# Optimization experiments

Hardware: AMD Instinct MI355X
Metric: run time of the kernel (lower is better)

Reference implementation:

```python
import jax, jax.numpy as jnp
import numpy as np

B, S, H = 2, 2048, 2048
N_HEADS = 16
HEAD_DIM = H // N_HEADS


def setup_inputs() -> dict:
    key = jax.random.key(0)
    ks = jax.random.split(key, 9)
    s = 1.0 / np.sqrt(H)
    inp = {
        "x": jax.random.normal(ks[0], (B, S, H), dtype=jnp.float32),
        "wq": jax.random.uniform(ks[1], (H, H), jnp.float32, -s, s),
        "bq": jnp.zeros((H,), jnp.float32),
        "wk": jax.random.uniform(ks[2], (H, H), jnp.float32, -s, s),
        "bk": jnp.zeros((H,), jnp.float32),
        "wv": jax.random.uniform(ks[3], (H, H), jnp.float32, -s, s),
        "bv": jnp.zeros((H,), jnp.float32),
        "wo": jax.random.uniform(ks[4], (H, H), jnp.float32, -s, s),
        "bo": jnp.zeros((H,), jnp.float32),
    }
    return inp


def reference(x, wq, bq, wk, bk, wv, bv, wo, bo):
    bsz, seq_len, hidden = x.shape
    scale = HEAD_DIM ** -0.5
    # projections -> [b, h, s, d]
    def proj(w, b):
        y = jnp.einsum("bsh,oh->bso", x, w) + b
        return y.reshape(bsz, seq_len, N_HEADS, HEAD_DIM).transpose(0, 2, 1, 3)
    q = proj(wq, bq)
    k = proj(wk, bk)
    v = proj(wv, bv)
    scores = jnp.einsum("bhqd,bhkd->bhqk", q, k) * scale
    causal = jnp.tril(jnp.ones((seq_len, seq_len), dtype=bool))
    scores = jnp.where(causal, scores, -jnp.inf)
    attn = jax.nn.softmax(scores, axis=-1)
    out = jnp.einsum("bhqk,bhkd->bhqd", attn, v)
    out = out.transpose(0, 2, 1, 3).reshape(bsz, seq_len, hidden)
    return jnp.einsum("bsh,oh->bso", out, wo) + bo
```

## Files before the change

kernel.cpp:

```cpp
#include <hip/hip_runtime.h>
#include <hip/hip_bf16.h>
#include <cstdint>
#include <cstddef>

#define BATCH 2
#define S_LEN 2048
#define HID   2048
#define NH    16
#define HD    128
#define GK    2048
#define NT    (GK / 64)
#define NIT   (NT / 2)
#define ATT_TILES (32 * NH * BATCH)

typedef short bf16x8 __attribute__((ext_vector_type(8)));
typedef float f32x4  __attribute__((ext_vector_type(4)));

__device__ inline unsigned short f2bf(float f) {
    unsigned int u = __float_as_uint(f);
    unsigned int r = (u + 0x7fffu + ((u >> 16) & 1u)) >> 16;
    return (unsigned short)r;
}

__global__ __launch_bounds__(256) void conv_f32_bf16(const float* __restrict__ src,
                                                     unsigned short* __restrict__ dst,
                                                     long n) {
    long i = ((long)blockIdx.x * 256 + threadIdx.x) * 8;
    if (i >= n) return;
    const float4 a = *(const float4*)(src + i);
    const float4 b = *(const float4*)(src + i + 4);
    union { unsigned short u[8]; bf16x8 v; } o;
    o.u[0] = f2bf(a.x); o.u[1] = f2bf(a.y); o.u[2] = f2bf(a.z); o.u[3] = f2bf(a.w);
    o.u[4] = f2bf(b.x); o.u[5] = f2bf(b.y); o.u[6] = f2bf(b.z); o.u[7] = f2bf(b.w);
    *(bf16x8*)(dst + i) = o.v;
}

__global__ __launch_bounds__(256) void conv4_f32_bf16(const float* __restrict__ s0,
                                                      const float* __restrict__ s1,
                                                      const float* __restrict__ s2,
                                                      const float* __restrict__ s3,
                                                      unsigned short* __restrict__ d0,
                                                      unsigned short* __restrict__ d1,
                                                      unsigned short* __restrict__ d2,
                                                      unsigned short* __restrict__ d3,
                                                      long n) {
    const int z = blockIdx.y;
    const float* src = (z == 0) ? s0 : (z == 1) ? s1 : (z == 2) ? s2 : s3;
    unsigned short* dst = (z == 0) ? d0 : (z == 1) ? d1 : (z == 2) ? d2 : d3;
    long i = ((long)blockIdx.x * 256 + threadIdx.x) * 8;
    if (i >= n) return;
    const float4 a = *(const float4*)(src + i);
    const float4 b = *(const float4*)(src + i + 4);
    union { unsigned short u[8]; bf16x8 v; } o;
    o.u[0] = f2bf(a.x); o.u[1] = f2bf(a.y); o.u[2] = f2bf(a.z); o.u[3] = f2bf(a.w);
    o.u[4] = f2bf(b.x); o.u[5] = f2bf(b.y); o.u[6] = f2bf(b.z); o.u[7] = f2bf(b.w);
    *(bf16x8*)(dst + i) = o.v;
}

__global__ void zero_int(int* p) { *p = 0; }


#define STAGE(DU, SRC, KT, H) do {                                            \
    const unsigned short* _s0 = (SRC) + (size_t)((H) * 128) * GK + (KT) * 64; \
    __builtin_amdgcn_global_load_lds(                                         \
        (const __attribute__((address_space(1))) void*)_s0,                   \
        (__attribute__((address_space(3))) void*)(Sm + (DU) + (H) * 8192 + sdst), \
        16, 0, 0);                                                            \
    __builtin_amdgcn_global_load_lds(                                         \
        (const __attribute__((address_space(1))) void*)(_s0 + (size_t)64 * GK), \
        (__attribute__((address_space(3))) void*)(Sm + (DU) + (H) * 8192 + 4096 + sdst), \
        16, 0, 0);                                                            \
} while (0)

#define READ_AF(D, AB) do { _Pragma("unroll")                                 \
    for (int mi = 0; mi < 4; ++mi) {                                          \
        const int r_ = wm * 64 + mi * 16 + ln;                                \
        AB[mi][0] = *(const bf16x8*)&Sm[(D) * 24576 + r_ * 64 + sw0];         \
        AB[mi][1] = *(const bf16x8*)&Sm[(D) * 24576 + r_ * 64 + sw1];         \
    } } while (0)

#define READ_BH(D, BB, HH) do { _Pragma("unroll")                             \
    for (int ni = 0; ni < 2; ++ni) {                                          \
        const int r_ = wn * 64 + ((HH) * 2 + ni) * 16 + ln;                   \
        BB[ni][0] = *(const bf16x8*)&Sm[(D) * 24576 + 16384 + r_ * 64 + sw0]; \
        BB[ni][1] = *(const bf16x8*)&Sm[(D) * 24576 + 16384 + r_ * 64 + sw1]; \
    } } while (0)

#define MFMA_H(AB, BB, HH) do { _Pragma("unroll")                             \
    for (int mi = 0; mi < 4; ++mi) _Pragma("unroll")                          \
    for (int ni = 0; ni < 2; ++ni) _Pragma("unroll")                          \
    for (int ks = 0; ks < 2; ++ks)                                            \
        acc[mi][(HH)*2+ni] = __builtin_amdgcn_mfma_f32_16x16x32_bf16(         \
            AB[mi][ks], BB[ni][ks], acc[mi][(HH)*2+ni], 0, 0, 0);             \
} while (0)

#define PRIO1 __builtin_amdgcn_s_setprio(1)
#define PRIO0 __builtin_amdgcn_s_setprio(0)
#define BAR   __builtin_amdgcn_s_barrier()
#define VM0   asm volatile("s_waitcnt vmcnt(0)" ::: "memory")

__device__ __forceinline__ void gemm256_core(const unsigned short* __restrict__ A,
                                             const unsigned short* __restrict__ Bw,
                                             const float* __restrict__ bias,
                                             void* __restrict__ Cout,
                                             int mode, int M0, int N0,
                                             unsigned short* Sm) {
    const int tid  = threadIdx.x;
    const int lane = tid & 63;
    const int wave = tid >> 6;
    const int ln = lane & 15, g = lane >> 4;
    const int wm = wave & 3, wn = wave >> 2;

    const int strow = tid >> 3;
    const int stcol = (((tid & 7) ^ ((tid >> 3) & 7)) << 3);
    const unsigned short* gA = A  + (size_t)(M0 + strow) * GK + stcol;
    const unsigned short* gB = Bw + (size_t)(N0 + strow) * GK + stcol;
    const int sdst = wave * 512;

    const int sw0 = ((g    ) ^ (ln & 7)) << 3;
    const int sw1 = ((g + 4) ^ (ln & 7)) << 3;

    f32x4 acc[4][4];
#pragma unroll
    for (int i = 0; i < 4; ++i)
#pragma unroll
        for (int j = 0; j < 4; ++j) acc[i][j] = (f32x4){0.f, 0.f, 0.f, 0.f};
    bf16x8 aE[4][2], aO[4][2], bA[2][2], bB[2][2];

    STAGE(0,     gA, 0, 0); STAGE(0,     gA, 0, 1);
    STAGE(16384, gB, 0, 0);
    STAGE(24576, gA, 1, 0); STAGE(24576, gA, 1, 1);
    asm volatile("s_waitcnt vmcnt(4)" ::: "memory");
    BAR;
    READ_AF(0, aE); READ_BH(0, bA, 0);

    for (int it = 0; it < NIT; ++it) {
        const int kt1 = 2 * it + 1;
        const int kt2 = (2 * it + 2 < NT) ? 2 * it + 2 : NT - 1;
        const int kt3 = (2 * it + 3 < NT) ? 2 * it + 3 : NT - 1;
        BAR;
        STAGE(24576 + 16384, gB, kt1, 0);
        READ_BH(0, bB, 1);
        PRIO1; MFMA_H(aE, bA, 0); PRIO0;
        VM0;
        BAR;
        STAGE(0, gA, kt2, 0); STAGE(0, gA, kt2, 1);
        READ_AF(1, aO); READ_BH(1, bA, 0);
        PRIO1; MFMA_H(aE, bB, 1); PRIO0;
        BAR;
        STAGE(16384, gB, kt2, 0);
        READ_BH(1, bB, 1);
        PRIO1; MFMA_H(aO, bA, 0); PRIO0;
        VM0;
        BAR;
        STAGE(24576, gA, kt3, 0); STAGE(24576, gA, kt3, 1);
        READ_AF(0, aE); READ_BH(0, bA, 0);
        PRIO1; MFMA_H(aO, bB, 1); PRIO0;
    }
    asm volatile("s_waitcnt vmcnt(0)" ::: "memory");
    __syncthreads();

    if (mode == 0) {
        const int bb = M0 >> 11;
        const int sb = M0 & (S_LEN - 1);
        const int h  = N0 >> 7;
#pragma unroll
        for (int nf = 0; nf < 4; ++nf) {
            const int d = wn * 64 + nf * 16 + ln;
            const float bn = bias[N0 + d];
            unsigned short* dst = (unsigned short*)Cout +
                (((size_t)(bb * NH + h) * S_LEN + sb + wm * 64) * HD + d);
#pragma unroll
            for (int mf = 0; mf < 4; ++mf)
#pragma unroll
                for (int r = 0; r < 4; ++r)
                    dst[(size_t)(mf * 16 + g * 4 + r) * HD] = f2bf(acc[mf][nf][r] + bn);
        }
    } else if (mode == 2) {
        float* dst = (float*)Cout;
#pragma unroll
        for (int nf = 0; nf < 4; ++nf) {
            const int n = N0 + wn * 64 + nf * 16 + ln;
            const float bn = bias[n];
#pragma unroll
            for (int mf = 0; mf < 4; ++mf)
#pragma unroll
                for (int r = 0; r < 4; ++r) {
                    const int m = M0 + wm * 64 + mf * 16 + g * 4 + r;
                    dst[(size_t)m * HID + n] = acc[mf][nf][r] + bn;
                }
        }
    } else {
        const int bb = M0 >> 11;
        const int sb = M0 & (S_LEN - 1);
        const int h  = N0 >> 7;
#pragma unroll
        for (int p = 0; p < 2; ++p) {
            if ((wm >> 1) == p) {
#pragma unroll
                for (int nf = 0; nf < 4; ++nf) {
                    const int dl = wn * 64 + nf * 16 + ln;
                    const float bn = bias[N0 + dl];
#pragma unroll
                    for (int mf = 0; mf < 4; ++mf) {
                        const int sl = (wm & 1) * 64 + mf * 16 + g * 4;
                        const int cs = (sl >> 3) ^ (dl & 15);
                        union { unsigned short u[4]; unsigned long long q; } pk;
#pragma unroll
                        for (int r = 0; r < 4; ++r) pk.u[r] = f2bf(acc[mf][nf][r] + bn);
                        *(unsigned long long*)&Sm[dl * 128 + cs * 8 + (sl & 7)] = pk.q;
                    }
                }
            }
            __syncthreads();
            {
                const int dl = tid >> 2;
                unsigned short* dst = (unsigned short*)Cout +
                    ((size_t)(bb * NH + h) * HD + dl) * S_LEN + sb + p * 128;
#pragma unroll
                for (int jj = 0; jj < 4; ++jj) {
                    const int sc = (tid & 3) + jj * 4;
                    const int cs = sc ^ (dl & 15);
                    *(bf16x8*)(dst + sc * 8) = *(const bf16x8*)&Sm[dl * 128 + cs * 8];
                }
            }
            __syncthreads();
        }
    }
}

__global__ __launch_bounds__(512, 2) void gemm_qkv256(
        const unsigned short* __restrict__ A,
        const unsigned short* __restrict__ w0, const unsigned short* __restrict__ w1,
        const unsigned short* __restrict__ w2,
        const float* __restrict__ b0, const float* __restrict__ b1,
        const float* __restrict__ b2,
        void* o0, void* o1, void* o2) {
    extern __shared__ __align__(16) unsigned short Sm[];
    const int z = blockIdx.z;
    const unsigned short* Bw = (z == 0) ? w0 : (z == 1) ? w1 : w2;
    const float* bias = (z == 0) ? b0 : (z == 1) ? b1 : b2;
    void* Cout = (z == 0) ? o0 : (z == 1) ? o1 : o2;
    gemm256_core(A, Bw, bias, Cout, (z == 2) ? 1 : 0,
                 blockIdx.y * 256, blockIdx.x * 128, Sm);
}

__global__ __launch_bounds__(512, 2) void gemm_out256(
        const unsigned short* __restrict__ A, const unsigned short* __restrict__ Bw,
        const float* __restrict__ bias, float* __restrict__ Cout) {
    extern __shared__ __align__(16) unsigned short Sm[];
    gemm256_core(A, Bw, bias, Cout, 2, blockIdx.y * 256, blockIdx.x * 128, Sm);
}

__global__ __launch_bounds__(256, 2) void attn_kernel(const unsigned short* __restrict__ Q,
                                                      const unsigned short* __restrict__ Kk,
                                                      const unsigned short* __restrict__ Vt,
                                                      unsigned short* __restrict__ O,
                                                      int* __restrict__ ticket) {
    __shared__ __align__(16) unsigned short Ks[2 * 64 * 128];
    __shared__ __align__(16) unsigned short Vs[2 * 128 * 64];
    __shared__ __align__(16) unsigned short Pl[4][16 * 72];
    __shared__ int tsh;
    const int tid = threadIdx.x;
    const int lane = tid & 63;
    const int wave = tid >> 6;
    const int g = lane >> 4, ln = lane & 15;
    const float scale2 = 0.08838834764831845f * 1.4426950408889634f;
    const bf16x8 ones_v = {0x3F80, 0x3F80, 0x3F80, 0x3F80, 0x3F80, 0x3F80, 0x3F80, 0x3F80};

    const int kcol = ((tid & 15) ^ ((tid >> 4) & 15)) * 8;
    const int vcol = ((tid & 7) ^ ((tid >> 3) & 7)) * 8;

    for (;;) {
        if (tid == 0) tsh = atomicAdd(ticket, 1);
        __syncthreads();
        const int t = tsh;
        if (t >= ATT_TILES) break;
        const int qt = 31 - (t >> 5);
        const int bh = t & 31;
        const int qbase = qt * 64 + wave * 16;

        const unsigned short* Qp = Q  + (size_t)bh * S_LEN * HD;
        const unsigned short* Kp = Kk + (size_t)bh * S_LEN * HD;
        const unsigned short* Vp = Vt + (size_t)bh * HD * S_LEN;

        bf16x8 aq[4];
#pragma unroll
        for (int dc = 0; dc < 4; ++dc)
            aq[dc] = *(const bf16x8*)&Qp[(size_t)(qbase + ln) * HD + dc * 32 + g * 8];

        f32x4 acc[9];
#pragma unroll
        for (int i = 0; i < 9; ++i) acc[i] = (f32x4){0.f, 0.f, 0.f, 0.f};

#pragma unroll
        for (int i = 0; i < 4; ++i) {
            const unsigned short* gk = Kp + (size_t)(i * 16 + (tid >> 4)) * HD + kcol;
            __builtin_amdgcn_global_load_lds(
                (const __attribute__((address_space(1))) void*)gk,
                (__attribute__((address_space(3))) void*)(Ks + i * 2048 + wave * 512),
                16, 0, 0);
        }
#pragma unroll
        for (int i = 0; i < 4; ++i) {
            const unsigned short* gv = Vp + (size_t)(i * 32 + (tid >> 3)) * S_LEN + vcol;
            __builtin_amdgcn_global_load_lds(
                (const __attribute__((address_space(1))) void*)gv,
                (__attribute__((address_space(3))) void*)(Vs + i * 2048 + wave * 512),
                16, 0, 0);
        }

        for (int kt = 0; kt <= qt; ++kt) {
            const int cur = kt & 1;
            const bool do_stage = (kt + 1 <= qt);
            if (do_stage) {
                const int kb2 = (kt + 1) * 64;
                const int nb  = (kt + 1) & 1;
                unsigned short* kdst = Ks + nb * 8192 + wave * 512;
                unsigned short* vdst = Vs + nb * 8192 + wave * 512;
#pragma unroll
                for (int i = 0; i < 4; ++i) {
                    const unsigned short* gk = Kp + (size_t)(kb2 + i * 16 + (tid >> 4)) * HD + kcol;
                    __builtin_amdgcn_global_load_lds(
                        (const __attribute__((address_space(1))) void*)gk,
                        (__attribute__((address_space(3))) void*)(kdst + i * 2048),
                        16, 0, 0);
                }
#pragma unroll
                for (int i = 0; i < 4; ++i) {
                    const unsigned short* gv = Vp + (size_t)(i * 32 + (tid >> 3)) * S_LEN + kb2 + vcol;
                    __builtin_amdgcn_global_load_lds(
                        (const __attribute__((address_space(1))) void*)gv,
                        (__attribute__((address_space(3))) void*)(vdst + i * 2048),
                        16, 0, 0);
                }
            }
            if (kt == 0 || !do_stage) {
                asm volatile("s_waitcnt vmcnt(0)" ::: "memory");
            } else {
                asm volatile("s_waitcnt vmcnt(8)" ::: "memory");
            }
            __builtin_amdgcn_s_barrier();

            const int kbuf = cur * 8192;
            f32x4 sc[4];
            __builtin_amdgcn_s_setprio(1);
#pragma unroll
            for (int nc = 0; nc < 4; ++nc) {
                sc[nc] = (f32x4){0.f, 0.f, 0.f, 0.f};
#pragma unroll
                for (int dc = 0; dc < 4; ++dc) {
                    bf16x8 bk = *(const bf16x8*)&Ks[kbuf + (nc * 16 + ln) * 128 + ((dc * 4 + g) ^ ln) * 8];
                    sc[nc] = __builtin_amdgcn_mfma_f32_16x16x32_bf16(aq[dc], bk, sc[nc], 0, 0, 0);
                }
            }
            __builtin_amdgcn_s_setprio(0);
            const bool diag = (kt == qt);
#pragma unroll
            for (int nc = 0; nc < 4; ++nc)
#pragma unroll
                for (int r = 0; r < 4; ++r) {
                    float pv = __builtin_amdgcn_exp2f(sc[nc][r] * scale2);
                    if (diag && (nc * 16 + ln > wave * 16 + g * 4 + r)) pv = 0.f;
                    Pl[wave][(g * 4 + r) * 72 + nc * 16 + ln] = f2bf(pv);
                }
            __builtin_amdgcn_s_setprio(1);
#pragma unroll
            for (int kc = 0; kc < 2; ++kc) {
                bf16x8 ap = *(const bf16x8*)&Pl[wave][ln * 72 + kc * 32 + g * 8];
#pragma unroll
                for (int d2 = 0; d2 < 8; ++d2) {
                    bf16x8 bv = *(const bf16x8*)&Vs[kbuf + (d2 * 16 + ln) * 64 + ((kc * 4 + g) ^ (ln & 7)) * 8];
                    acc[d2] = __builtin_amdgcn_mfma_f32_16x16x32_bf16(ap, bv, acc[d2], 0, 0, 0);
                }
                acc[8] = __builtin_amdgcn_mfma_f32_16x16x32_bf16(ap, ones_v, acc[8], 0, 0, 0);
            }
            __builtin_amdgcn_s_setprio(0);
            __builtin_amdgcn_s_barrier();
        }
        const int b = bh >> 4, h = bh & 15;
        float inv[4];
#pragma unroll
        for (int r = 0; r < 4; ++r) inv[r] = 1.0f / acc[8][r];
#pragma unroll
        for (int d2 = 0; d2 < 8; ++d2)
#pragma unroll
            for (int r = 0; r < 4; ++r) {
                const int row = qbase + g * 4 + r;
                const int col = h * HD + d2 * 16 + ln;
                O[((size_t)b * S_LEN + row) * HID + col] = f2bf(acc[d2][r] * inv[r]);
            }
    }
}

extern "C" void kernel_launch(void* const* d_in, const int* in_sizes, int n_in,
                              void* d_out, int out_size, void* d_ws, size_t ws_size,
                              hipStream_t stream) {
    const float* x  = (const float*)d_in[0];
    const float* wq = (const float*)d_in[1];
    const float* bq = (const float*)d_in[2];
    const float* wk = (const float*)d_in[3];
    const float* bk = (const float*)d_in[4];
    const float* wv = (const float*)d_in[5];
    const float* bv = (const float*)d_in[6];
    const float* wo = (const float*)d_in[7];
    const float* bo = (const float*)d_in[8];
    float* out = (float*)d_out;

    const long nx = (long)BATCH * S_LEN * HID;
    const long nw = (long)HID * HID;

    char* p = (char*)d_ws;
    unsigned short* xb  = (unsigned short*)p; p += nx * 2;
    unsigned short* wqb = (unsigned short*)p; p += nw * 2;
    unsigned short* wkb = (unsigned short*)p; p += nw * 2;
    unsigned short* wvb = (unsigned short*)p; p += nw * 2;
    unsigned short* wob = (unsigned short*)p; p += nw * 2;
    unsigned short* Qb  = (unsigned short*)p; p += nx * 2;
    unsigned short* Kb  = (unsigned short*)p; p += nx * 2;
    unsigned short* Vtb = (unsigned short*)p; p += nx * 2;
    unsigned short* Ob  = (unsigned short*)p; p += nx * 2;
    int* ticket = (int*)p;

    conv_f32_bf16<<<(int)(nx / 8 / 256), 256, 0, stream>>>(x, xb, nx);
    dim3 cgrid((unsigned)(nw / 8 / 256), 4);
    conv4_f32_bf16<<<cgrid, 256, 0, stream>>>(wq, wk, wv, wo, wqb, wkb, wvb, wob, nw);
    zero_int<<<1, 1, 0, stream>>>(ticket);

    const int M = BATCH * S_LEN;
    dim3 qkvgrid(HID / 128, M / 256, 3);
    gemm_qkv256<<<qkvgrid, 512, 98304, stream>>>(xb, wqb, wkb, wvb, bq, bk, bv,
                                                 Qb, Kb, Vtb);

    attn_kernel<<<512, 256, 0, stream>>>(Qb, Kb, Vtb, Ob, ticket);

    dim3 ogrid(HID / 128, M / 256);
    gemm_out256<<<ogrid, 512, 98304, stream>>>(Ob, wob, bo, out);
}
```

Measured before the change: 378.9 us.

## Double attention query tile to 128 rows so each wave computes two 16-row blocks

The attention kernel now processes 128 query rows per tile, with each wave handling two 16-row MFMA blocks. Each K/V tile loaded into LDS is therefore reused across twice as many queries, halving K/V global traffic per query. The persistent grid is halved to 256 blocks and launch bounds drop to one block per SIMD group. The cost is double the accumulator registers, lower occupancy, coarser causal load balancing with fewer tiles, and two masked diagonal sub-tiles per tile.

```diff
diff --git a/kernel.cpp b/kernel.cpp
--- a/kernel.cpp
+++ b/kernel.cpp
@@ -11,7 +11,7 @@
 #define GK    2048
 #define NT    (GK / 64)
 #define NIT   (NT / 2)
-#define ATT_TILES (32 * NH * BATCH)
+#define ATT_TILES2 (16 * NH * BATCH)
 
 typedef short bf16x8 __attribute__((ext_vector_type(8)));
 typedef float f32x4  __attribute__((ext_vector_type(4)));
@@ -252,14 +252,14 @@
     gemm256_core(A, Bw, bias, Cout, 2, blockIdx.y * 256, blockIdx.x * 128, Sm);
 }
 
-__global__ __launch_bounds__(256, 2) void attn_kernel(const unsigned short* __restrict__ Q,
+__global__ __launch_bounds__(256, 1) void attn_kernel(const unsigned short* __restrict__ Q,
                                                       const unsigned short* __restrict__ Kk,
                                                       const unsigned short* __restrict__ Vt,
                                                       unsigned short* __restrict__ O,
                                                       int* __restrict__ ticket) {
     __shared__ __align__(16) unsigned short Ks[2 * 64 * 128];
     __shared__ __align__(16) unsigned short Vs[2 * 128 * 64];
-    __shared__ __align__(16) unsigned short Pl[4][16 * 72];
+    __shared__ __align__(16) unsigned short Pl[4][32 * 72];
     __shared__ int tsh;
     const int tid = threadIdx.x;
     const int lane = tid & 63;
@@ -275,23 +275,27 @@
         if (tid == 0) tsh = atomicAdd(ticket, 1);
         __syncthreads();
         const int t = tsh;
-        if (t >= ATT_TILES) break;
-        const int qt = 31 - (t >> 5);
+        if (t >= ATT_TILES2) break;
+        const int qt = 15 - (t >> 5);
         const int bh = t & 31;
-        const int qbase = qt * 64 + wave * 16;
+        const int qbase = qt * 128 + wave * 32;
 
         const unsigned short* Qp = Q  + (size_t)bh * S_LEN * HD;
         const unsigned short* Kp = Kk + (size_t)bh * S_LEN * HD;
         const unsigned short* Vp = Vt + (size_t)bh * HD * S_LEN;
 
-        bf16x8 aq[4];
-#pragma unroll
-        for (int dc = 0; dc < 4; ++dc)
-            aq[dc] = *(const bf16x8*)&Qp[(size_t)(qbase + ln) * HD + dc * 32 + g * 8];
-
-        f32x4 acc[9];
-#pragma unroll
-        for (int i = 0; i < 9; ++i) acc[i] = (f32x4){0.f, 0.f, 0.f, 0.f};
+        bf16x8 aq[2][4];
+#pragma unroll
+        for (int mi = 0; mi < 2; ++mi)
+#pragma unroll
+            for (int dc = 0; dc < 4; ++dc)
+                aq[mi][dc] = *(const bf16x8*)&Qp[(size_t)(qbase + mi * 16 + ln) * HD + dc * 32 + g * 8];
+
+        f32x4 acc[2][9];
+#pragma unroll
+        for (int mi = 0; mi < 2; ++mi)
+#pragma unroll
+            for (int i = 0; i < 9; ++i) acc[mi][i] = (f32x4){0.f, 0.f, 0.f, 0.f};
 
 #pragma unroll
         for (int i = 0; i < 4; ++i) {
@@ -310,9 +314,10 @@
                 16, 0, 0);
         }
 
-        for (int kt = 0; kt <= qt; ++kt) {
+        const int ktmax = 2 * qt + 1;
+        for (int kt = 0; kt <= ktmax; ++kt) {
             const int cur = kt & 1;
-            const bool do_stage = (kt + 1 <= qt);
+            const bool do_stage = (kt < ktmax);
             if (do_stage) {
                 const int kb2 = (kt + 1) * 64;
                 const int nb  = (kt + 1) & 1;
@@ -343,53 +348,66 @@
             __builtin_amdgcn_s_barrier();
 
             const int kbuf = cur * 8192;
-            f32x4 sc[4];
+            f32x4 sc[2][4];
             __builtin_amdgcn_s_setprio(1);
 #pragma unroll
             for (int nc = 0; nc < 4; ++nc) {
-                sc[nc] = (f32x4){0.f, 0.f, 0.f, 0.f};
+                sc[0][nc] = (f32x4){0.f, 0.f, 0.f, 0.f};
+                sc[1][nc] = (f32x4){0.f, 0.f, 0.f, 0.f};
 #pragma unroll
                 for (int dc = 0; dc < 4; ++dc) {
                     bf16x8 bk = *(const bf16x8*)&Ks[kbuf + (nc * 16 + ln) * 128 + ((dc * 4 + g) ^ ln) * 8];
-                    sc[nc] = __builtin_amdgcn_mfma_f32_16x16x32_bf16(aq[dc], bk, sc[nc], 0, 0, 0);
+                    sc[0][nc] = __builtin_amdgcn_mfma_f32_16x16x32_bf16(aq[0][dc], bk, sc[0][nc], 0, 0, 0);
+                    sc[1][nc] = __builtin_amdgcn_mfma_f32_16x16x32_bf16(aq[1][dc], bk, sc[1][nc], 0, 0, 0);
                 }
             }
             __builtin_amdgcn_s_setprio(0);
-            const bool diag = (kt == qt);
-#pragma unroll
-            for (int nc = 0; nc < 4; ++nc)
-#pragma unroll
-                for (int r = 0; r < 4; ++r) {
-                    float pv = __builtin_amdgcn_exp2f(sc[nc][r] * scale2);
-                    if (diag && (nc * 16 + ln > wave * 16 + g * 4 + r)) pv = 0.f;
-                    Pl[wave][(g * 4 + r) * 72 + nc * 16 + ln] = f2bf(pv);
-                }
+            const int krel = kt - 2 * qt;
+#pragma unroll
+            for (int mi = 0; mi < 2; ++mi)
+#pragma unroll
+                for (int nc = 0; nc < 4; ++nc)
+#pragma unroll
+                    for (int r = 0; r < 4; ++r) {
+                        float pv = __builtin_amdgcn_exp2f(sc[mi][nc][r] * scale2);
+                        if (krel >= 0 &&
+                            (krel * 64 + nc * 16 + ln > wave * 32 + mi * 16 + g * 4 + r))
+                            pv = 0.f;
+                        Pl[wave][(mi * 16 + g * 4 + r) * 72 + nc * 16 + ln] = f2bf(pv);
+                    }
             __builtin_amdgcn_s_setprio(1);
 #pragma unroll
             for (int kc = 0; kc < 2; ++kc) {
-                bf16x8 ap = *(const bf16x8*)&Pl[wave][ln * 72 + kc * 32 + g * 8];
+                bf16x8 ap0 = *(const bf16x8*)&Pl[wave][(     ln) * 72 + kc * 32 + g * 8];
+                bf16x8 ap1 = *(const bf16x8*)&Pl[wave][(16 + ln) * 72 + kc * 32 + g * 8];
 #pragma unroll
                 for (int d2 = 0; d2 < 8; ++d2) {
                     bf16x8 bv = *(const bf16x8*)&Vs[kbuf + (d2 * 16 + ln) * 64 + ((kc * 4 + g) ^ (ln & 7)) * 8];
-                    acc[d2] = __builtin_amdgcn_mfma_f32_16x16x32_bf16(ap, bv, acc[d2], 0, 0, 0);
-                }
-                acc[8] = __builtin_amdgcn_mfma_f32_16x16x32_bf16(ap, ones_v, acc[8], 0, 0, 0);
+                    acc[0][d2] = __builtin_amdgcn_mfma_f32_16x16x32_bf16(ap0, bv, acc[0][d2], 0, 0, 0);
+                    acc[1][d2] = __builtin_amdgcn_mfma_f32_16x16x32_bf16(ap1, bv, acc[1][d2], 0, 0, 0);
+                }
+                acc[0][8] = __builtin_amdgcn_mfma_f32_16x16x32_bf16(ap0, ones_v, acc[0][8], 0, 0, 0);
+                acc[1][8] = __builtin_amdgcn_mfma_f32_16x16x32_bf16(ap1, ones_v, acc[1][8], 0, 0, 0);
             }
             __builtin_amdgcn_s_setprio(0);
             __builtin_amdgcn_s_barrier();
         }
         const int b = bh >> 4, h = bh & 15;
-        float inv[4];
-#pragma unroll
-        for (int r = 0; r < 4; ++r) inv[r] = 1.0f / acc[8][r];
-#pragma unroll
-        for (int d2 = 0; d2 < 8; ++d2)
-#pragma unroll
-            for (int r = 0; r < 4; ++r) {
-                const int row = qbase + g * 4 + r;
-                const int col = h * HD + d2 * 16 + ln;
-                O[((size_t)b * S_LEN + row) * HID + col] = f2bf(acc[d2][r] * inv[r]);
-            }
+        float inv[2][4];
+#pragma unroll
+        for (int mi = 0; mi < 2; ++mi)
+#pragma unroll
+            for (int r = 0; r < 4; ++r) inv[mi][r] = 1.0f / acc[mi][8][r];
+#pragma unroll
+        for (int mi = 0; mi < 2; ++mi)
+#pragma unroll
+            for (int d2 = 0; d2 < 8; ++d2)
+#pragma unroll
+                for (int r = 0; r < 4; ++r) {
+                    const int row = qbase + mi * 16 + g * 4 + r;
+                    const int col = h * HD + d2 * 16 + ln;
+                    O[((size_t)b * S_LEN + row) * HID + col] = f2bf(acc[mi][d2][r] * inv[mi][r]);
+                }
     }
 }
 
@@ -432,7 +450,7 @@
     gemm_qkv256<<<qkvgrid, 512, 98304, stream>>>(xb, wqb, wkb, wvb, bq, bk, bv,
                                                  Qb, Kb, Vtb);
 
-    attn_kernel<<<512, 256, 0, stream>>>(Qb, Kb, Vtb, Ob, ticket);
+    attn_kernel<<<256, 256, 0, stream>>>(Qb, Kb, Vtb, Ob, ticket);
 
     dim3 ogrid(HID / 128, M / 256);
     gemm_out256<<<ogrid, 512, 98304, stream>>>(Ob, wob, bo, out);
```

New measurement: 394.8 us. +4.2%, slower.
